# Optimization experiments

Hardware: AMD Instinct MI355X
Metric: run time of the kernel (lower is better)

Reference implementation:

```python
import jax, jax.numpy as jnp
import numpy as np

SIGMA = 0.05  # gaussian bandwidth from the source


def _sqdist(a, b):
    # a: [B,N,D], b: [B,M,D] -> [B,N,M] squared euclidean distance
    a2 = jnp.sum(a * a, axis=-1)[:, :, None]
    b2 = jnp.sum(b * b, axis=-1)[:, None, :]
    return a2 + b2 - 2.0 * jnp.einsum('bnd,bmd->bnm', a, b)


def setup_inputs() -> dict:
    key = jax.random.key(0)
    k1, k2, k3, k4 = jax.random.split(key, 4)
    B, N, D = 2, 4096, 32
    points = jax.random.normal(k1, (B, N, 3), dtype=jnp.float32)
    pointfea1 = jax.random.normal(k2, (B, N, D), dtype=jnp.float32)
    pointfea2 = jax.random.normal(k3, (B, N, D), dtype=jnp.float32)
    weights = jax.random.uniform(k4, (B, N), dtype=jnp.float32) / N  # point-cloud mass weights
    return {"points": points, "pointfea1": pointfea1, "pointfea2": pointfea2, "weights": weights}


def reference(points, pointfea1, pointfea2, weights):
    # naive_corres: per-point spatial log-gaussian softmax vs feature log-softmax,
    # weighted squared difference, reduced over both pair axes -> [B]
    x = points / SIGMA
    point_loggauss = jax.nn.log_softmax(-_sqdist(x, x), axis=2)          # [B,N,N]
    fea_logsoftmax = jax.nn.log_softmax(-_sqdist(pointfea1, pointfea2), axis=2)  # [B,N,N]
    diff2 = (jnp.exp(point_loggauss) - jnp.exp(fea_logsoftmax)) ** 2
    l2_loss = jnp.sum(diff2 * weights[:, :, None], axis=2)  # sum over j
    return jnp.sum(l2_loss, axis=1)                          # sum over i -> [B]
```

## Files before the change

kernel.cpp:

```cpp
#include <hip/hip_runtime.h>

#define D    32
#define BLK  256
#define NCH  16
#define LOG2E 1.44269504088896340736f

typedef short  short8  __attribute__((ext_vector_type(8)));
typedef float  floatx4 __attribute__((ext_vector_type(4)));
typedef float  v2f     __attribute__((ext_vector_type(2)));

__device__ __forceinline__ short f2bf(float v) {
    union { float f; unsigned u; } x; x.f = v;
    unsigned r = x.u + 0x7fffu + ((x.u >> 16) & 1u);
    return (short)(r >> 16);
}
__device__ __forceinline__ float bf2f(short h) {
    union { float f; unsigned u; } x;
    x.u = ((unsigned)(unsigned short)h) << 16;
    return x.f;
}
__device__ __forceinline__ float fast_exp2(float x) {
#if __has_builtin(__builtin_amdgcn_exp2f)
    return __builtin_amdgcn_exp2f(x);
#else
    return exp2f(x);
#endif
}

__global__ __launch_bounds__(BLK) void precompute_kernel(
    const float* __restrict__ points,
    const float* __restrict__ fea1,
    const float* __restrict__ fea2,
    float4* __restrict__ xp,
    float* __restrict__ f1n,
    float* __restrict__ f2n,
    short* __restrict__ f1hi,
    short* __restrict__ f1lo,
    short* __restrict__ f2hi,
    short* __restrict__ f2lo,
    float* __restrict__ acc,
    float* __restrict__ out,
    int BN, int Bsz)
{
    int r = blockIdx.x * BLK + threadIdx.x;
    if (r < Bsz) out[r] = 0.0f;
    if (r >= BN) return;
#pragma unroll
    for (int s = 0; s < 5; ++s) acc[s * BN + r] = 0.0f;

    const float s20 = 20.0f;
    float x = points[3*r+0] * s20;
    float y = points[3*r+1] * s20;
    float z = points[3*r+2] * s20;
    float4 v; v.x = x; v.y = y; v.z = z;
    v.w = (x*x + y*y + z*z) * LOG2E;
    xp[r] = v;

    const int t = r >> 4;
    const int m = r & 15;
    const float* p1 = fea1 + (size_t)r * D;
    const float* p2 = fea2 + (size_t)r * D;
    float n1 = 0.f, n2 = 0.f;
#pragma unroll
    for (int q = 0; q < 4; ++q) {
        size_t off = ((size_t)t * 64 + m + 16*q) * 8;
        float4 a0 = *(const float4*)(p1 + q*8);
        float4 a1 = *(const float4*)(p1 + q*8 + 4);
        float e1[8] = {a0.x,a0.y,a0.z,a0.w,a1.x,a1.y,a1.z,a1.w};
        short8 h1, l1;
#pragma unroll
        for (int k = 0; k < 8; ++k) {
            n1 = fmaf(e1[k], e1[k], n1);
            short hh = f2bf(e1[k]);
            h1[k] = hh;
            l1[k] = f2bf(e1[k] - bf2f(hh));
        }
        *(short8*)&f1hi[off] = h1;
        *(short8*)&f1lo[off] = l1;

        float4 b0 = *(const float4*)(p2 + q*8);
        float4 b1 = *(const float4*)(p2 + q*8 + 4);
        float e2[8] = {b0.x,b0.y,b0.z,b0.w,b1.x,b1.y,b1.z,b1.w};
        short8 h2, l2;
#pragma unroll
        for (int k = 0; k < 8; ++k) {
            n2 = fmaf(e2[k], e2[k], n2);
            short hh = f2bf(e2[k]);
            h2[k] = hh;
            l2[k] = f2bf(e2[k] - bf2f(hh));
        }
        *(short8*)&f2hi[off] = h2;
        *(short8*)&f2lo[off] = l2;
    }
    f1n[r] = n1 * LOG2E;
    f2n[r] = n2 * LOG2E;
}

__global__ __launch_bounds__(BLK) void pair_kernel(
    const short* __restrict__ f1hi,
    const short* __restrict__ f1lo,
    const short* __restrict__ f2hi,
    const short* __restrict__ f2lo,
    const float4* __restrict__ xp,
    const float* __restrict__ f1n,
    const float* __restrict__ f2n,
    float* __restrict__ acc,
    int N, int BN)
{
    const int tid  = threadIdx.x;
    const int lane = tid & 63;
    const int wv   = tid >> 6;
    const int m    = lane & 15;
    const int q    = lane >> 4;

    const int ibpb  = N >> 6;
    const int b     = blockIdx.x / ibpb;
    const int ibase = blockIdx.x << 6;
    const int JCH   = N / NCH;
    const int jc0   = blockIdx.y * JCH;

    const float L2 = 2.0f * LOG2E;

    short8 Bh[4], Bl[4];
    float xsx[4], xsy[4], xsz[4], mw[4], nf[4];
#pragma unroll
    for (int it = 0; it < 4; ++it) {
        size_t ti = ((size_t)(blockIdx.x * 4 + it) * 64 + lane) * 8;
        Bh[it] = *(const short8*)&f1hi[ti];
        Bl[it] = *(const short8*)&f1lo[ti];
        int irow = ibase + it*16 + m;
        float4 xi = xp[irow];
        xsx[it] = xi.x * L2; xsy[it] = xi.y * L2; xsz[it] = xi.z * L2;
        mw[it] = -xi.w;
        nf[it] = -f1n[irow];
    }

    v2f  sAB[4] = {{0.f,0.f},{0.f,0.f},{0.f,0.f},{0.f,0.f}};
    v2f  s2 [4] = {{0.f,0.f},{0.f,0.f},{0.f,0.f},{0.f,0.f}};
    float sab[4] = {0.f,0.f,0.f,0.f};

    const int ntw    = JCH >> 6;
    const int tjbase = (b * N + jc0) >> 4;

    for (int t = 0; t < ntw; ++t) {
        const int jt = wv * ntw + t;
        const size_t tj = ((size_t)(tjbase + jt) * 64 + lane) * 8;
        short8 Ah = *(const short8*)&f2hi[tj];
        short8 Al = *(const short8*)&f2lo[tj];

        const int jb = b * N + jc0 + jt * 16 + q * 4;
        float4 xjv[4];
        xjv[0] = xp[jb+0]; xjv[1] = xp[jb+1]; xjv[2] = xp[jb+2]; xjv[3] = xp[jb+3];
        floatx4 fnr = *(const floatx4*)&f2n[jb];

#pragma unroll
        for (int it = 0; it < 4; ++it) {
            floatx4 c = {0.f, 0.f, 0.f, 0.f};
            c = __builtin_amdgcn_mfma_f32_16x16x32_bf16(Ah, Bh[it], c, 0, 0, 0);
            c = __builtin_amdgcn_mfma_f32_16x16x32_bf16(Ah, Bl[it], c, 0, 0, 0);
            c = __builtin_amdgcn_mfma_f32_16x16x32_bf16(Al, Bh[it], c, 0, 0, 0);
#pragma unroll
            for (int r = 0; r < 4; ++r) {
                float aL = fmaf(xsz[it], xjv[r].z,
                             fmaf(xsy[it], xjv[r].y,
                              fmaf(xsx[it], xjv[r].x, mw[it]))) - xjv[r].w;
                float bL = fmaf(c[r], L2, nf[it] - fnr[r]);
                float ea = fast_exp2(aL);
                float eb = fast_exp2(bL);
                v2f e = {ea, eb};
                sAB[it] += e;
                s2[it]   = __builtin_elementwise_fma(e, e, s2[it]);
                sab[it]  = fmaf(ea, eb, sab[it]);
            }
        }
    }

#pragma unroll
    for (int it = 0; it < 4; ++it) {
        float vA = sAB[it].x, vB = sAB[it].y;
        float v2a = s2[it].x, v2b = s2[it].y, vab = sab[it];
        vA  += __shfl_xor(vA, 16);  vA  += __shfl_xor(vA, 32);
        vB  += __shfl_xor(vB, 16);  vB  += __shfl_xor(vB, 32);
        v2a += __shfl_xor(v2a, 16); v2a += __shfl_xor(v2a, 32);
        v2b += __shfl_xor(v2b, 16); v2b += __shfl_xor(v2b, 32);
        vab += __shfl_xor(vab, 16); vab += __shfl_xor(vab, 32);
        if (lane < 16) {
            int row = ibase + it*16 + lane;
            atomicAdd(&acc[0*BN + row], vA);
            atomicAdd(&acc[1*BN + row], v2a);
            atomicAdd(&acc[2*BN + row], vB);
            atomicAdd(&acc[3*BN + row], v2b);
            atomicAdd(&acc[4*BN + row], vab);
        }
    }
}

__global__ __launch_bounds__(BLK) void finalize_kernel(
    const float* __restrict__ acc,
    const float* __restrict__ weights,
    float* __restrict__ out,
    int N, int BN)
{
    int row = blockIdx.x * BLK + threadIdx.x;
    int b   = (blockIdx.x * BLK) / N;

    float A   = acc[0*BN + row];
    float S2a = acc[1*BN + row];
    float Bt  = acc[2*BN + row];
    float S2b = acc[3*BN + row];
    float Sab = acc[4*BN + row];
    float invA = 1.0f / A;
    float invB = 1.0f / Bt;
    float val  = S2a*invA*invA - 2.0f*Sab*invA*invB + S2b*invB*invB;
    float sum  = weights[row] * val;

    __shared__ float red[BLK/64];
    for (int off = 32; off > 0; off >>= 1)
        sum += __shfl_down(sum, off);
    if ((threadIdx.x & 63) == 0) red[threadIdx.x >> 6] = sum;
    __syncthreads();
    if (threadIdx.x == 0) {
        float s = 0.f;
#pragma unroll
        for (int w = 0; w < BLK/64; ++w) s += red[w];
        atomicAdd(&out[b], s);
    }
}

extern "C" void kernel_launch(void* const* d_in, const int* in_sizes, int n_in,
                              void* d_out, int out_size, void* d_ws, size_t ws_size,
                              hipStream_t stream) {
    const float* points  = (const float*)d_in[0];
    const float* fea1    = (const float*)d_in[1];
    const float* fea2    = (const float*)d_in[2];
    const float* weights = (const float*)d_in[3];
    float* out = (float*)d_out;

    int B  = out_size;
    int BN = in_sizes[3];
    int N  = BN / B;

    float*  acc  = (float*)d_ws;
    float4* xp   = (float4*)((char*)d_ws + (size_t)5  * BN * 4);
    float*  f2n  = (float*)((char*)d_ws + (size_t)9  * BN * 4);
    float*  f1n  = (float*)((char*)d_ws + (size_t)10 * BN * 4);
    short*  f1hi = (short*)((char*)d_ws + (size_t)11 * BN * 4);
    short*  f1lo = f1hi + (size_t)BN * D;
    short*  f2hi = f1lo + (size_t)BN * D;
    short*  f2lo = f2hi + (size_t)BN * D;

    precompute_kernel<<<dim3((BN + BLK - 1) / BLK), dim3(BLK), 0, stream>>>(
        points, fea1, fea2, xp, f1n, f2n, f1hi, f1lo, f2hi, f2lo, acc, out, BN, B);

    dim3 grid(BN / 64, NCH);
    pair_kernel<<<grid, dim3(BLK), 0, stream>>>(
        f1hi, f1lo, f2hi, f2lo, xp, f1n, f2n, acc, N, BN);

    finalize_kernel<<<dim3(BN / BLK), dim3(BLK), 0, stream>>>(acc, weights, out, N, BN);
}
```

Baseline: 90.66 us.

## Compute spatial gaussian logits via MFMA and stage j-tiles through LDS

The spatial squared-distance term is now encoded as a split-bf16 (hi/lo/lo-lo) dot product with the norms folded in, so a single MFMA produces the exp2 argument instead of per-element FMAs. The feature logits use the MFMA accumulator initialised with the norm offsets, which removes the post-MFMA FMA. The j-side operands are loaded cooperatively into shared memory and shared across four waves, each wave owning one i-tile instead of four. NCH is halved, giving fewer, longer blocks. The trade-offs are an extra sync per stage, lower register-level reuse of the i operands, and bf16-split precision on the spatial distances.

```diff
diff --git a/kernel.cpp b/kernel.cpp
--- a/kernel.cpp
+++ b/kernel.cpp
@@ -2,12 +2,13 @@
 
 #define D    32
 #define BLK  256
-#define NCH  16
+#define NCH  8
+#define STJ  64
 #define LOG2E 1.44269504088896340736f
 
-typedef short  short8  __attribute__((ext_vector_type(8)));
-typedef float  floatx4 __attribute__((ext_vector_type(4)));
-typedef float  v2f     __attribute__((ext_vector_type(2)));
+typedef short short8  __attribute__((ext_vector_type(8)));
+typedef float floatx4 __attribute__((ext_vector_type(4)));
+typedef float v2f     __attribute__((ext_vector_type(2)));
 
 __device__ __forceinline__ short f2bf(float v) {
     union { float f; unsigned u; } x; x.f = v;
@@ -31,15 +32,11 @@
     const float* __restrict__ points,
     const float* __restrict__ fea1,
     const float* __restrict__ fea2,
-    float4* __restrict__ xp,
-    float* __restrict__ f1n,
-    float* __restrict__ f2n,
-    short* __restrict__ f1hi,
-    short* __restrict__ f1lo,
-    short* __restrict__ f2hi,
-    short* __restrict__ f2lo,
-    float* __restrict__ acc,
-    float* __restrict__ out,
+    short* __restrict__ sAj, short* __restrict__ sBi,
+    short* __restrict__ fAh, short* __restrict__ fAl,
+    short* __restrict__ fBh, short* __restrict__ fBl,
+    float* __restrict__ fn2, float* __restrict__ nf1,
+    float* __restrict__ acc, float* __restrict__ out,
     int BN, int Bsz)
 {
     int r = blockIdx.x * BLK + threadIdx.x;
@@ -48,65 +45,102 @@
 #pragma unroll
     for (int s = 0; s < 5; ++s) acc[s * BN + r] = 0.0f;
 
-    const float s20 = 20.0f;
-    float x = points[3*r+0] * s20;
-    float y = points[3*r+1] * s20;
-    float z = points[3*r+2] * s20;
-    float4 v; v.x = x; v.y = y; v.z = z;
-    v.w = (x*x + y*y + z*z) * LOG2E;
-    xp[r] = v;
-
-    const int t = r >> 4;
-    const int m = r & 15;
+    const float s2l = sqrtf(2.0f * LOG2E);
+    const int t = r >> 4, m = r & 15;
+    const size_t fb = ((size_t)t * 64 + m) * 8;
+
+    float x0 = points[3*r+0] * 20.f;
+    float x1 = points[3*r+1] * 20.f;
+    float x2 = points[3*r+2] * 20.f;
+    float xn = (x0*x0 + x1*x1 + x2*x2) * LOG2E;
+    float xs[3] = {x0*s2l, x1*s2l, x2*s2l};
+    short h[3], l[3], ll[3];
+#pragma unroll
+    for (int c = 0; c < 3; ++c) {
+        h[c] = f2bf(xs[c]);
+        float rm = xs[c] - bf2f(h[c]);
+        l[c] = f2bf(rm);
+        rm -= bf2f(l[c]);
+        ll[c] = f2bf(rm);
+    }
+    short xnh = f2bf(xn);
+    float rn = xn - bf2f(xnh);
+    short xnm = f2bf(rn);
+    rn -= bf2f(xnm);
+    short xnl = f2bf(rn);
+    const short N1 = (short)0xBF80;
+
+    short8 aq[4], bq[4];
+    aq[0] = (short8){h[0],h[1],h[2], l[0],l[1],l[2], ll[0],ll[1]};
+    aq[1] = (short8){ll[2], h[0],h[1],h[2], l[0],l[1],l[2], ll[0]};
+    aq[2] = (short8){ll[1],ll[2], h[0],h[1],h[2], l[0],l[1],l[2]};
+    aq[3] = (short8){ll[0],ll[1],ll[2], xnh,xnm,xnl, N1,N1};
+    bq[0] = (short8){h[0],h[1],h[2], h[0],h[1],h[2], h[0],h[1]};
+    bq[1] = (short8){h[2], l[0],l[1],l[2], l[0],l[1],l[2], l[0]};
+    bq[2] = (short8){l[1],l[2], ll[0],ll[1],ll[2], ll[0],ll[1],ll[2]};
+    bq[3] = (short8){ll[0],ll[1],ll[2], N1,N1,N1, xnh,xnm};
+#pragma unroll
+    for (int q = 0; q < 4; ++q) {
+        *(short8*)&sAj[fb + q*128] = aq[q];
+        *(short8*)&sBi[fb + q*128] = bq[q];
+    }
+
     const float* p1 = fea1 + (size_t)r * D;
     const float* p2 = fea2 + (size_t)r * D;
     float n1 = 0.f, n2 = 0.f;
 #pragma unroll
     for (int q = 0; q < 4; ++q) {
-        size_t off = ((size_t)t * 64 + m + 16*q) * 8;
         float4 a0 = *(const float4*)(p1 + q*8);
         float4 a1 = *(const float4*)(p1 + q*8 + 4);
         float e1[8] = {a0.x,a0.y,a0.z,a0.w,a1.x,a1.y,a1.z,a1.w};
-        short8 h1, l1;
+        short8 hh1, ll1;
 #pragma unroll
         for (int k = 0; k < 8; ++k) {
             n1 = fmaf(e1[k], e1[k], n1);
-            short hh = f2bf(e1[k]);
-            h1[k] = hh;
-            l1[k] = f2bf(e1[k] - bf2f(hh));
+            float v = e1[k] * s2l;
+            short hv = f2bf(v);
+            hh1[k] = hv;
+            ll1[k] = f2bf(v - bf2f(hv));
         }
-        *(short8*)&f1hi[off] = h1;
-        *(short8*)&f1lo[off] = l1;
+        *(short8*)&fBh[fb + q*128] = hh1;
+        *(short8*)&fBl[fb + q*128] = ll1;
 
         float4 b0 = *(const float4*)(p2 + q*8);
         float4 b1 = *(const float4*)(p2 + q*8 + 4);
         float e2[8] = {b0.x,b0.y,b0.z,b0.w,b1.x,b1.y,b1.z,b1.w};
-        short8 h2, l2;
+        short8 hh2, ll2;
 #pragma unroll
         for (int k = 0; k < 8; ++k) {
             n2 = fmaf(e2[k], e2[k], n2);
-            short hh = f2bf(e2[k]);
-            h2[k] = hh;
-            l2[k] = f2bf(e2[k] - bf2f(hh));
+            float v = e2[k] * s2l;
+            short hv = f2bf(v);
+            hh2[k] = hv;
+            ll2[k] = f2bf(v - bf2f(hv));
         }
-        *(short8*)&f2hi[off] = h2;
-        *(short8*)&f2lo[off] = l2;
-    }
-    f1n[r] = n1 * LOG2E;
-    f2n[r] = n2 * LOG2E;
+        *(short8*)&fAh[fb + q*128] = hh2;
+        *(short8*)&fAl[fb + q*128] = ll2;
+    }
+    nf1[r] = n1 * LOG2E;
+    fn2[r] = n2 * LOG2E;
 }
 
 __global__ __launch_bounds__(BLK) void pair_kernel(
-    const short* __restrict__ f1hi,
-    const short* __restrict__ f1lo,
-    const short* __restrict__ f2hi,
-    const short* __restrict__ f2lo,
-    const float4* __restrict__ xp,
-    const float* __restrict__ f1n,
-    const float* __restrict__ f2n,
+    const short* __restrict__ sAj,
+    const short* __restrict__ fAh,
+    const short* __restrict__ fAl,
+    const short* __restrict__ sBi,
+    const short* __restrict__ fBh,
+    const short* __restrict__ fBl,
+    const float* __restrict__ fn2,
+    const float* __restrict__ nf1,
     float* __restrict__ acc,
     int N, int BN)
 {
+    __shared__ __align__(16) short lAs[STJ * D];
+    __shared__ __align__(16) short lAh[STJ * D];
+    __shared__ __align__(16) short lAl[STJ * D];
+    __shared__ float lFn[STJ];
+
     const int tid  = threadIdx.x;
     const int lane = tid & 63;
     const int wv   = tid >> 6;
@@ -115,83 +149,76 @@
 
     const int ibpb  = N >> 6;
     const int b     = blockIdx.x / ibpb;
-    const int ibase = blockIdx.x << 6;
+    const int itile = blockIdx.x * 4 + wv;
     const int JCH   = N / NCH;
     const int jc0   = blockIdx.y * JCH;
 
-    const float L2 = 2.0f * LOG2E;
-
-    short8 Bh[4], Bl[4];
-    float xsx[4], xsy[4], xsz[4], mw[4], nf[4];
-#pragma unroll
-    for (int it = 0; it < 4; ++it) {
-        size_t ti = ((size_t)(blockIdx.x * 4 + it) * 64 + lane) * 8;
-        Bh[it] = *(const short8*)&f1hi[ti];
-        Bl[it] = *(const short8*)&f1lo[ti];
-        int irow = ibase + it*16 + m;
-        float4 xi = xp[irow];
-        xsx[it] = xi.x * L2; xsy[it] = xi.y * L2; xsz[it] = xi.z * L2;
-        mw[it] = -xi.w;
-        nf[it] = -f1n[irow];
-    }
-
-    v2f  sAB[4] = {{0.f,0.f},{0.f,0.f},{0.f,0.f},{0.f,0.f}};
-    v2f  s2 [4] = {{0.f,0.f},{0.f,0.f},{0.f,0.f},{0.f,0.f}};
-    float sab[4] = {0.f,0.f,0.f,0.f};
-
-    const int ntw    = JCH >> 6;
+    const size_t ti = ((size_t)itile * 64 + lane) * 8;
+    short8 Bs  = *(const short8*)&sBi[ti];
+    short8 Bfh = *(const short8*)&fBh[ti];
+    short8 Bfl = *(const short8*)&fBl[ti];
+    float nfin = -nf1[itile * 16 + m];
+
+    v2f  sAB = {0.f, 0.f};
+    v2f  s2  = {0.f, 0.f};
+    float sab = 0.f;
+
     const int tjbase = (b * N + jc0) >> 4;
-
-    for (int t = 0; t < ntw; ++t) {
-        const int jt = wv * ntw + t;
-        const size_t tj = ((size_t)(tjbase + jt) * 64 + lane) * 8;
-        short8 Ah = *(const short8*)&f2hi[tj];
-        short8 Al = *(const short8*)&f2lo[tj];
-
-        const int jb = b * N + jc0 + jt * 16 + q * 4;
-        float4 xjv[4];
-        xjv[0] = xp[jb+0]; xjv[1] = xp[jb+1]; xjv[2] = xp[jb+2]; xjv[3] = xp[jb+3];
-        floatx4 fnr = *(const floatx4*)&f2n[jb];
-
-#pragma unroll
-        for (int it = 0; it < 4; ++it) {
-            floatx4 c = {0.f, 0.f, 0.f, 0.f};
-            c = __builtin_amdgcn_mfma_f32_16x16x32_bf16(Ah, Bh[it], c, 0, 0, 0);
-            c = __builtin_amdgcn_mfma_f32_16x16x32_bf16(Ah, Bl[it], c, 0, 0, 0);
-            c = __builtin_amdgcn_mfma_f32_16x16x32_bf16(Al, Bh[it], c, 0, 0, 0);
+    const short* gAs = sAj + (size_t)tjbase * 512;
+    const short* gAh = fAh + (size_t)tjbase * 512;
+    const short* gAl = fAl + (size_t)tjbase * 512;
+    const float* gFn = fn2 + (size_t)b * N + jc0;
+
+    for (int s0 = 0; s0 < JCH; s0 += STJ) {
+        const int to = s0 * 4;
+        ((uint4*)lAs)[tid] = ((const uint4*)gAs)[to + tid];
+        ((uint4*)lAh)[tid] = ((const uint4*)gAh)[to + tid];
+        ((uint4*)lAl)[tid] = ((const uint4*)gAl)[to + tid];
+        if (tid < STJ) lFn[tid] = gFn[s0 + tid];
+        __syncthreads();
+
+#pragma unroll 2
+        for (int tt = 0; tt < STJ/16; ++tt) {
+            const short8 As = *(const short8*)&lAs[(tt*64 + lane)*8];
+            const short8 Ah = *(const short8*)&lAh[(tt*64 + lane)*8];
+            const short8 Al = *(const short8*)&lAl[(tt*64 + lane)*8];
+            floatx4 fnq = *(const floatx4*)&lFn[tt*16 + q*4];
+
+            floatx4 cs = {0.f, 0.f, 0.f, 0.f};
+            cs = __builtin_amdgcn_mfma_f32_16x16x32_bf16(As, Bs, cs, 0, 0, 0);
+
+            floatx4 cf = {nfin - fnq[0], nfin - fnq[1],
+                          nfin - fnq[2], nfin - fnq[3]};
+            cf = __builtin_amdgcn_mfma_f32_16x16x32_bf16(Ah, Bfh, cf, 0, 0, 0);
+            cf = __builtin_amdgcn_mfma_f32_16x16x32_bf16(Ah, Bfl, cf, 0, 0, 0);
+            cf = __builtin_amdgcn_mfma_f32_16x16x32_bf16(Al, Bfh, cf, 0, 0, 0);
+
 #pragma unroll
             for (int r = 0; r < 4; ++r) {
-                float aL = fmaf(xsz[it], xjv[r].z,
-                             fmaf(xsy[it], xjv[r].y,
-                              fmaf(xsx[it], xjv[r].x, mw[it]))) - xjv[r].w;
-                float bL = fmaf(c[r], L2, nf[it] - fnr[r]);
-                float ea = fast_exp2(aL);
-                float eb = fast_exp2(bL);
+                float ea = fast_exp2(cs[r]);
+                float eb = fast_exp2(cf[r]);
                 v2f e = {ea, eb};
-                sAB[it] += e;
-                s2[it]   = __builtin_elementwise_fma(e, e, s2[it]);
-                sab[it]  = fmaf(ea, eb, sab[it]);
+                sAB += e;
+                s2   = __builtin_elementwise_fma(e, e, s2);
+                sab  = fmaf(ea, eb, sab);
             }
         }
-    }
-
-#pragma unroll
-    for (int it = 0; it < 4; ++it) {
-        float vA = sAB[it].x, vB = sAB[it].y;
-        float v2a = s2[it].x, v2b = s2[it].y, vab = sab[it];
-        vA  += __shfl_xor(vA, 16);  vA  += __shfl_xor(vA, 32);
-        vB  += __shfl_xor(vB, 16);  vB  += __shfl_xor(vB, 32);
-        v2a += __shfl_xor(v2a, 16); v2a += __shfl_xor(v2a, 32);
-        v2b += __shfl_xor(v2b, 16); v2b += __shfl_xor(v2b, 32);
-        vab += __shfl_xor(vab, 16); vab += __shfl_xor(vab, 32);
-        if (lane < 16) {
-            int row = ibase + it*16 + lane;
-            atomicAdd(&acc[0*BN + row], vA);
-            atomicAdd(&acc[1*BN + row], v2a);
-            atomicAdd(&acc[2*BN + row], vB);
-            atomicAdd(&acc[3*BN + row], v2b);
-            atomicAdd(&acc[4*BN + row], vab);
-        }
+        __syncthreads();
+    }
+
+    float vA = sAB.x, vB = sAB.y, v2a = s2.x, v2b = s2.y, vab = sab;
+    vA  += __shfl_xor(vA, 16);  vA  += __shfl_xor(vA, 32);
+    vB  += __shfl_xor(vB, 16);  vB  += __shfl_xor(vB, 32);
+    v2a += __shfl_xor(v2a, 16); v2a += __shfl_xor(v2a, 32);
+    v2b += __shfl_xor(v2b, 16); v2b += __shfl_xor(v2b, 32);
+    vab += __shfl_xor(vab, 16); vab += __shfl_xor(vab, 32);
+    if (lane < 16) {
+        int row = itile * 16 + lane;
+        atomicAdd(&acc[0*BN + row], vA);
+        atomicAdd(&acc[1*BN + row], v2a);
+        atomicAdd(&acc[2*BN + row], vB);
+        atomicAdd(&acc[3*BN + row], v2b);
+        atomicAdd(&acc[4*BN + row], vab);
     }
 }
 
@@ -240,21 +267,24 @@
     int BN = in_sizes[3];
     int N  = BN / B;
 
-    float*  acc  = (float*)d_ws;
-    float4* xp   = (float4*)((char*)d_ws + (size_t)5  * BN * 4);
-    float*  f2n  = (float*)((char*)d_ws + (size_t)9  * BN * 4);
-    float*  f1n  = (float*)((char*)d_ws + (size_t)10 * BN * 4);
-    short*  f1hi = (short*)((char*)d_ws + (size_t)11 * BN * 4);
-    short*  f1lo = f1hi + (size_t)BN * D;
-    short*  f2hi = f1lo + (size_t)BN * D;
-    short*  f2lo = f2hi + (size_t)BN * D;
+    float* acc = (float*)d_ws;
+    char*  p   = (char*)d_ws + (size_t)5 * BN * 4;
+    short* sAj = (short*)p; p += (size_t)BN * 64;
+    short* sBi = (short*)p; p += (size_t)BN * 64;
+    short* fAh = (short*)p; p += (size_t)BN * 64;
+    short* fAl = (short*)p; p += (size_t)BN * 64;
+    short* fBh = (short*)p; p += (size_t)BN * 64;
+    short* fBl = (short*)p; p += (size_t)BN * 64;
+    float* fn2 = (float*)p; p += (size_t)BN * 4;
+    float* nf1 = (float*)p;
 
     precompute_kernel<<<dim3((BN + BLK - 1) / BLK), dim3(BLK), 0, stream>>>(
-        points, fea1, fea2, xp, f1n, f2n, f1hi, f1lo, f2hi, f2lo, acc, out, BN, B);
+        points, fea1, fea2, sAj, sBi, fAh, fAl, fBh, fBl, fn2, nf1,
+        acc, out, BN, B);
 
     dim3 grid(BN / 64, NCH);
     pair_kernel<<<grid, dim3(BLK), 0, stream>>>(
-        f1hi, f1lo, f2hi, f2lo, xp, f1n, f2n, acc, N, BN);
+        sAj, fAh, fAl, sBi, fBh, fBl, fn2, nf1, acc, N, BN);
 
     finalize_kernel<<<dim3(BN / BLK), dim3(BLK), 0, stream>>>(acc, weights, out, N, BN);
 }
```

Measured after the change: 86.74 us. 1.05x faster.
